# Kernel tuning notes

Hardware: AMD Instinct MI355X
Metric: run time of the kernel (lower is better)

Reference implementation:

```python
import jax, jax.numpy as jnp
import numpy as np

B, N, T, M, D, H = 2, 2048, 8, 256, 1024, 16
HD = D // H
EPS = 1e-5


def setup_inputs() -> dict:
    key = jax.random.key(0)
    ks = jax.random.split(key, 12)
    text_tokens = jax.random.normal(ks[0], (B, N, D), dtype=jnp.float32)
    media = jax.random.normal(ks[1], (B, T, M, D), dtype=jnp.float32)
    # exactly T media markers, evenly spaced, first at position 0 so no
    # fully-masked softmax row (matches well-formed usage of the module)
    loc = np.zeros((B, N), dtype=bool)
    loc[:, (np.arange(T) * (N // T))] = True
    media_locations = jnp.asarray(loc)
    s = 0.02
    return {
        "text_tokens": text_tokens,
        "media": media,
        "media_locations": media_locations,
        "ln_gamma": jnp.ones((D,), jnp.float32),
        "ln_beta": jnp.zeros((D,), jnp.float32),
        "wq": jax.random.normal(ks[2], (D, D), jnp.float32) * s,
        "wk": jax.random.normal(ks[3], (D, D), jnp.float32) * s,
        "wv": jax.random.normal(ks[4], (D, D), jnp.float32) * s,
        "bq": jnp.zeros((D,), jnp.float32),
        "bk": jnp.zeros((D,), jnp.float32),
        "bv": jnp.zeros((D,), jnp.float32),
        "w_out": jax.random.normal(ks[5], (D, D), jnp.float32) * s,
        "b_out": jnp.zeros((D,), jnp.float32),
    }


def _layernorm(x, gamma, beta):
    mu = jnp.mean(x, axis=-1, keepdims=True)
    var = jnp.mean(jnp.square(x - mu), axis=-1, keepdims=True)
    return (x - mu) * jax.lax.rsqrt(var + EPS) * gamma + beta


def reference(text_tokens, media, media_locations, ln_gamma, ln_beta,
              wq, wk, wv, bq, bk, bv, w_out, b_out):
    b, t, m, d = media.shape
    n = text_tokens.shape[1]
    h, hd = H, HD

    x = _layernorm(text_tokens, ln_gamma, ln_beta)          # [b,n,d]
    kv = media.reshape(b, t * m, d)                          # [b,tm,d]

    q = (x @ wq + bq).reshape(b, n, h, hd)
    k = (kv @ wk + bk).reshape(b, t * m, h, hd)
    v = (kv @ wv + bv).reshape(b, t * m, h, hd)

    scale = 1.0 / jnp.sqrt(jnp.asarray(hd, jnp.float32))
    scores = jnp.einsum('bnhk,bshk->bhns', q, k) * scale     # [b,h,n,tm]

    # media-locality mask: text token attends only to its immediately
    # preceding media frame (cumsum of media_locations == frame index)
    text_cumsum = jnp.cumsum(media_locations.astype(jnp.int32), axis=-1)  # [b,n]
    media_nums = jnp.repeat(jnp.arange(1, t + 1, dtype=jnp.int32), m)     # [tm]
    allowed = text_cumsum[:, :, None] == media_nums[None, None, :]        # [b,n,tm]
    scores = jnp.where(allowed[:, None, :, :], scores, -jnp.inf)

    attn = jax.nn.softmax(scores, axis=-1)                   # [b,h,n,tm]
    out = jnp.einsum('bhns,bshk->bnhk', attn, v).reshape(b, n, d)
    return out @ w_out + b_out
```

## Files before the change

kernel.cpp:

```cpp
#include <hip/hip_runtime.h>
#include <hip/hip_fp16.h>


typedef _Float16 h8 __attribute__((ext_vector_type(8)));
typedef _Float16 h4 __attribute__((ext_vector_type(4)));
typedef float f4 __attribute__((ext_vector_type(4)));

#define DI __device__ __forceinline__

DI void gload16(const void* g, void* l) {
  __builtin_amdgcn_global_load_lds((const __attribute__((address_space(1))) unsigned int*)g,
                                   (__attribute__((address_space(3))) unsigned int*)l, 16, 0, 0);
}

#define BAR() do { asm volatile("" ::: "memory"); __builtin_amdgcn_s_barrier(); asm volatile("" ::: "memory"); } while (0)

__global__ __launch_bounds__(256) void prep_kernel(
    const float* __restrict__ x, const float* __restrict__ gamma, const float* __restrict__ beta,
    _Float16* __restrict__ xh,
    const float* __restrict__ media, _Float16* __restrict__ kvh,
    const float* __restrict__ W0, const float* __restrict__ W1,
    const float* __restrict__ W2, const float* __restrict__ W3, _Float16* __restrict__ Wt,
    const int* __restrict__ locs, int* __restrict__ cnt, int* __restrict__ qlist) {
  int bid = blockIdx.x;
  int tid = threadIdx.x;
  if (bid < 4096) {
    int row = bid;
    const f4* xr = (const f4*)(x + (size_t)row * 1024);
    f4 v = xr[tid];
    float s = v[0] + v[1] + v[2] + v[3];
    float ss = v[0]*v[0] + v[1]*v[1] + v[2]*v[2] + v[3]*v[3];
    #pragma unroll
    for (int m = 1; m < 64; m <<= 1) { s += __shfl_xor(s, m); ss += __shfl_xor(ss, m); }
    __shared__ float red[8];
    int wid = tid >> 6, lane = tid & 63;
    if (lane == 0) { red[wid] = s; red[4 + wid] = ss; }
    __syncthreads();
    s = red[0] + red[1] + red[2] + red[3];
    ss = red[4] + red[5] + red[6] + red[7];
    float mean = s * (1.0f / 1024.0f);
    float var = ss * (1.0f / 1024.0f) - mean * mean;
    float rs = rsqrtf(var + 1e-5f);
    f4 g = ((const f4*)gamma)[tid], be = ((const f4*)beta)[tid];
    h4 o;
    #pragma unroll
    for (int j = 0; j < 4; ++j) o[j] = (_Float16)((v[j] - mean) * rs * g[j] + be[j]);
    ((h4*)(xh + (size_t)row * 1024))[tid] = o;
  } else if (bid < 8192) {
    int i = (bid - 4096) * 256 + tid;
    f4 v = ((const f4*)media)[i];
    h4 o;
    #pragma unroll
    for (int j = 0; j < 4; ++j) o[j] = (_Float16)v[j];
    ((h4*)kvh)[i] = o;
  } else if (bid < 12288) {
    int sec = bid - 8192;
    int z = sec >> 10, r = sec & 1023;
    const float* W = z == 0 ? W0 : z == 1 ? W1 : z == 2 ? W2 : W3;
    _Float16* out = Wt + (size_t)z * 1024 * 1024;
    __shared__ float tile[32][33];
    int i0 = (r & 31) * 32, o0 = (r >> 5) * 32;
    int tx = tid & 31, ty = tid >> 5;
    #pragma unroll
    for (int rr = 0; rr < 4; ++rr)
      tile[ty + rr * 8][tx] = W[(size_t)(i0 + ty + rr * 8) * 1024 + o0 + tx];
    __syncthreads();
    #pragma unroll
    for (int rr = 0; rr < 4; ++rr)
      out[(size_t)(o0 + ty + rr * 8) * 1024 + i0 + tx] = (_Float16)tile[tx][ty + rr * 8];
  } else {
    int b = bid - 12288;
    __shared__ int lcnt[8];
    if (tid < 8) lcnt[tid] = 0;
    __syncthreads();
    if (tid < 64) {
      int lane = tid;
      int run = 0; int v[32];
      #pragma unroll
      for (int i = 0; i < 32; ++i) { run += locs[b * 2048 + lane * 32 + i]; v[i] = run; }
      int incl = run;
      #pragma unroll
      for (int d = 1; d < 64; d <<= 1) { int t = __shfl_up(incl, d); if (lane >= d) incl += t; }
      int excl = incl - run;
      #pragma unroll
      for (int i = 0; i < 32; ++i) {
        int c = excl + v[i];
        if (c >= 1 && c <= 8) {
          int pos = atomicAdd(&lcnt[c - 1], 1);
          qlist[(b * 8 + (c - 1)) * 2048 + pos] = lane * 32 + i;
        }
      }
    }
    __syncthreads();
    if (tid < 8) cnt[b * 8 + tid] = lcnt[tid];
  }
}

struct GemmDesc { const _Float16* A; const _Float16* Bt; const float* bias; void* C; int mode; };
struct GemmBatch { GemmDesc d[3]; };

__global__ __launch_bounds__(512, 2) void gemm256(GemmBatch gb) {
  GemmDesc g = gb.d[blockIdx.z];
  int row0 = blockIdx.y * 256, col0 = blockIdx.x * 256;
  __shared__ alignas(16) _Float16 As[2][256 * 64];
  __shared__ alignas(16) _Float16 Bs[2][256 * 64];
  int tid = threadIdx.x, lane = tid & 63, wid = tid >> 6;
  int wr = wid >> 2, wc = wid & 3;
  int rs = tid >> 3;
  int cg = (tid & 7) ^ (rs & 7);
  const _Float16* gA = g.A + (size_t)(row0 + rs) * 1024 + cg * 8;
  const _Float16* gB = g.Bt + (size_t)(col0 + rs) * 1024 + cg * 8;
  int dstoff = wid * 8 * 64;
  f4 acc[8][4] = {};

  auto STAGE = [&](int kt, int buf) {
    #pragma unroll
    for (int s = 0; s < 4; ++s) {
      gload16(gA + (size_t)s * 65536 + kt * 64, (void*)&As[buf][s * 4096 + dstoff]);
      gload16(gB + (size_t)s * 65536 + kt * 64, (void*)&Bs[buf][s * 4096 + dstoff]);
    }
  };
  STAGE(0, 0);
  int c0 = (lane >> 4) ^ (lane & 7);
  int c1 = (4 + (lane >> 4)) ^ (lane & 7);
  #pragma unroll 1
  for (int t = 0; t < 16; ++t) {
    int buf = t & 1;
    BAR();
    if (t < 15) {
      STAGE(t + 1, buf ^ 1);
      asm volatile("s_waitcnt vmcnt(8)" ::: "memory");
    } else {
      asm volatile("s_waitcnt vmcnt(0)" ::: "memory");
    }
    BAR();
    #pragma unroll
    for (int kk = 0; kk < 2; ++kk) {
      int cc = kk ? c1 : c0;
      h8 a[8], b[4];
      #pragma unroll
      for (int m = 0; m < 8; ++m)
        a[m] = *(const h8*)&As[buf][(wr * 128 + m * 16 + (lane & 15)) * 64 + cc * 8];
      #pragma unroll
      for (int n = 0; n < 4; ++n)
        b[n] = *(const h8*)&Bs[buf][(wc * 64 + n * 16 + (lane & 15)) * 64 + cc * 8];
      __builtin_amdgcn_s_setprio(1);
      #pragma unroll
      for (int m = 0; m < 8; ++m)
        #pragma unroll
        for (int n = 0; n < 4; ++n)
          acc[m][n] = __builtin_amdgcn_mfma_f32_16x16x32_f16(a[m], b[n], acc[m][n], 0, 0, 0);
      __builtin_amdgcn_s_setprio(0);
    }
  }
  int colb = col0 + wc * 64;
  float bias_v[4];
  #pragma unroll
  for (int n = 0; n < 4; ++n) bias_v[n] = g.bias[colb + n * 16 + (lane & 15)];
  #pragma unroll
  for (int m = 0; m < 8; ++m) {
    int row = row0 + wr * 128 + m * 16 + (lane >> 4) * 4;
    #pragma unroll
    for (int n = 0; n < 4; ++n) {
      int col = colb + n * 16 + (lane & 15);
      if (g.mode == 0) {
        _Float16* C = (_Float16*)g.C;
        #pragma unroll
        for (int j = 0; j < 4; ++j)
          C[(size_t)(row + j) * 1024 + col] = (_Float16)(acc[m][n][j] + bias_v[n]);
      } else if (g.mode == 1) {
        float* C = (float*)g.C;
        #pragma unroll
        for (int j = 0; j < 4; ++j)
          C[(size_t)(row + j) * 1024 + col] = acc[m][n][j] + bias_v[n];
      } else {
        _Float16* C = (_Float16*)g.C;
        h4 pk;
        #pragma unroll
        for (int j = 0; j < 4; ++j) pk[j] = (_Float16)(acc[m][n][j] + bias_v[n]);
        size_t vrow = (size_t)((row >> 11) * 1024 + col);
        *(h4*)&C[vrow * 2048 + (row & 2047)] = pk;
      }
    }
  }
}

__global__ __launch_bounds__(512) void gemm128(GemmBatch gb) {
  GemmDesc g = gb.d[blockIdx.z];
  int row0 = blockIdx.y * 128, col0 = blockIdx.x * 128;
  __shared__ alignas(16) _Float16 As[128 * 64];
  __shared__ alignas(16) _Float16 Bs[128 * 64];
  int tid = threadIdx.x, lane = tid & 63, wid = tid >> 6;
  int wr = wid >> 2, wc = wid & 3;
  f4 acc[4][2] = {};
  int r0s = tid >> 3, c0s = tid & 7;
  int cg0 = c0s ^ (r0s & 7);
  int r1s = r0s + 64;
  int cg1 = c0s ^ (r1s & 7);
  const _Float16* gA0 = g.A + (size_t)(row0 + r0s) * 1024 + cg0 * 8;
  const _Float16* gA1 = g.A + (size_t)(row0 + r1s) * 1024 + cg1 * 8;
  const _Float16* gB0 = g.Bt + (size_t)(col0 + r0s) * 1024 + cg0 * 8;
  const _Float16* gB1 = g.Bt + (size_t)(col0 + r1s) * 1024 + cg1 * 8;
  #pragma unroll 1
  for (int kt = 0; kt < 16; ++kt) {
    __syncthreads();
    gload16(gA0 + kt * 64, (void*)&As[wid * 512]);
    gload16(gA1 + kt * 64, (void*)&As[4096 + wid * 512]);
    gload16(gB0 + kt * 64, (void*)&Bs[wid * 512]);
    gload16(gB1 + kt * 64, (void*)&Bs[4096 + wid * 512]);
    __syncthreads();
    h8 af[2][4], bf[2][2];
    #pragma unroll
    for (int kk = 0; kk < 2; ++kk) {
      #pragma unroll
      for (int m = 0; m < 4; ++m) {
        int r = wr * 64 + m * 16 + (lane & 15);
        int c = ((lane >> 4) + kk * 4) ^ (r & 7);
        af[kk][m] = *(const h8*)&As[r * 64 + c * 8];
      }
      #pragma unroll
      for (int n = 0; n < 2; ++n) {
        int r = wc * 32 + n * 16 + (lane & 15);
        int c = ((lane >> 4) + kk * 4) ^ (r & 7);
        bf[kk][n] = *(const h8*)&Bs[r * 64 + c * 8];
      }
    }
    #pragma unroll
    for (int kk = 0; kk < 2; ++kk)
      #pragma unroll
      for (int m = 0; m < 4; ++m)
        #pragma unroll
        for (int n = 0; n < 2; ++n)
          acc[m][n] = __builtin_amdgcn_mfma_f32_16x16x32_f16(af[kk][m], bf[kk][n], acc[m][n], 0, 0, 0);
  }
  int colb = col0 + wc * 32;
  float bias_v[2];
  #pragma unroll
  for (int n = 0; n < 2; ++n) bias_v[n] = g.bias[colb + n * 16 + (lane & 15)];
  #pragma unroll
  for (int m = 0; m < 4; ++m) {
    int row = row0 + wr * 64 + m * 16 + (lane >> 4) * 4;
    #pragma unroll
    for (int n = 0; n < 2; ++n) {
      int col = colb + n * 16 + (lane & 15);
      if (g.mode == 0) {
        _Float16* C = (_Float16*)g.C;
        #pragma unroll
        for (int j = 0; j < 4; ++j)
          C[(size_t)(row + j) * 1024 + col] = (_Float16)(acc[m][n][j] + bias_v[n]);
      } else if (g.mode == 1) {
        float* C = (float*)g.C;
        #pragma unroll
        for (int j = 0; j < 4; ++j)
          C[(size_t)(row + j) * 1024 + col] = acc[m][n][j] + bias_v[n];
      } else {
        _Float16* C = (_Float16*)g.C;
        h4 pk;
        #pragma unroll
        for (int j = 0; j < 4; ++j) pk[j] = (_Float16)(acc[m][n][j] + bias_v[n]);
        size_t vrow = (size_t)((row >> 11) * 1024 + col);
        *(h4*)&C[vrow * 2048 + (row & 2047)] = pk;
      }
    }
  }
}

__global__ __launch_bounds__(512) void attn_kernel(const _Float16* __restrict__ Qg,
    const _Float16* __restrict__ Kg, const _Float16* __restrict__ Vtg,
    const int* __restrict__ cnt, const int* __restrict__ qlist, _Float16* __restrict__ Og) {
  int h = blockIdx.x, f = blockIdx.y, b = blockIdx.z;
  __shared__ alignas(16) _Float16 Kl[256 * 64];
  __shared__ alignas(16) _Float16 Vl[64 * 256];
  __shared__ alignas(16) _Float16 Sl[8 * 16 * 256];
  int tid = threadIdx.x;
  for (int idx = tid; idx < 2048; idx += 512) {
    int r = idx >> 3, c = idx & 7;
    h8 v = *(const h8*)&Kg[((size_t)(b * 2048 + f * 256 + r)) * 1024 + h * 64 + c * 8];
    *(h8*)&Kl[r * 64 + ((c ^ (r & 7)) * 8)] = v;
  }
  for (int idx = tid; idx < 2048; idx += 512) {
    int d = idx >> 5, cc = idx & 31;
    h8 v = *(const h8*)&Vtg[((size_t)(b * 1024 + h * 64 + d)) * 2048 + f * 256 + cc * 8];
    *(h8*)&Vl[d * 256 + ((cc ^ (d & 7)) * 8)] = v;
  }
  __syncthreads();
  int nq = cnt[b * 8 + f];
  int lane = tid & 63, wid = tid >> 6;
  const int* ql = qlist + (b * 8 + f) * 2048;
  _Float16* Sw = &Sl[wid * 4096];
  for (int st = wid; st * 16 < nq; st += 8) {
    int qbase = st * 16;
    int nv = nq - qbase; if (nv > 16) nv = 16;
    int li = lane & 15; if (li > nv - 1) li = nv - 1;
    int qrow = b * 2048 + ql[qbase + li];
    h8 aq0 = *(const h8*)&Qg[(size_t)qrow * 1024 + h * 64 + (lane >> 4) * 8];
    h8 aq1 = *(const h8*)&Qg[(size_t)qrow * 1024 + h * 64 + 32 + (lane >> 4) * 8];
    f4 s[16];
    #pragma unroll
    for (int kt = 0; kt < 16; ++kt) {
      int key = kt * 16 + (lane & 15);
      int cb0 = lane >> 4;
      h8 bk0 = *(const h8*)&Kl[key * 64 + ((cb0 ^ (key & 7)) * 8)];
      h8 bk1 = *(const h8*)&Kl[key * 64 + (((cb0 + 4) ^ (key & 7)) * 8)];
      f4 z = {0.f, 0.f, 0.f, 0.f};
      s[kt] = __builtin_amdgcn_mfma_f32_16x16x32_f16(aq0, bk0, z, 0, 0, 0);
      s[kt] = __builtin_amdgcn_mfma_f32_16x16x32_f16(aq1, bk1, s[kt], 0, 0, 0);
    }
    float mx[4], sm[4];
    #pragma unroll
    for (int j = 0; j < 4; ++j) {
      float m = s[0][j];
      #pragma unroll
      for (int kt = 1; kt < 16; ++kt) m = fmaxf(m, s[kt][j]);
      #pragma unroll
      for (int d = 1; d < 16; d <<= 1) m = fmaxf(m, __shfl_xor(m, d));
      mx[j] = m; sm[j] = 0.f;
    }
    #pragma unroll
    for (int kt = 0; kt < 16; ++kt) {
      int keyb = kt * 16 + (lane & 15);
      int cbk = keyb >> 3, wi = keyb & 7;
      #pragma unroll
      for (int j = 0; j < 4; ++j) {
        float p = __expf((s[kt][j] - mx[j]) * 0.125f);
        sm[j] += p;
        int q = (lane >> 4) * 4 + j;
        Sw[q * 256 + ((cbk ^ (q & 7)) * 8) + wi] = (_Float16)p;
      }
    }
    #pragma unroll
    for (int j = 0; j < 4; ++j) {
      float x = sm[j];
      #pragma unroll
      for (int d = 1; d < 16; d <<= 1) x += __shfl_xor(x, d);
      sm[j] = x;
    }
    f4 o[4] = {};
    #pragma unroll
    for (int c32 = 0; c32 < 8; ++c32) {
      int qa = lane & 15;
      int cba = c32 * 4 + (lane >> 4);
      h8 pa = *(const h8*)&Sw[qa * 256 + ((cba ^ (qa & 7)) * 8)];
      #pragma unroll
      for (int dt = 0; dt < 4; ++dt) {
        int dd = dt * 16 + (lane & 15);
        h8 bv_ = *(const h8*)&Vl[dd * 256 + ((cba ^ (dd & 7)) * 8)];
        o[dt] = __builtin_amdgcn_mfma_f32_16x16x32_f16(pa, bv_, o[dt], 0, 0, 0);
      }
    }
    #pragma unroll
    for (int j = 0; j < 4; ++j) {
      int q = (lane >> 4) * 4 + j;
      if (q < nv) {
        int qr = __shfl(qrow, q);
        float inv = 1.0f / sm[j];
        #pragma unroll
        for (int dt = 0; dt < 4; ++dt)
          Og[(size_t)qr * 1024 + h * 64 + dt * 16 + (lane & 15)] = (_Float16)(o[dt][j] * inv);
      }
    }
  }
}

extern "C" void kernel_launch(void* const* d_in, const int* in_sizes, int n_in,
                              void* d_out, int out_size, void* d_ws, size_t ws_size,
                              hipStream_t stream) {
  const float* text  = (const float*)d_in[0];
  const float* media = (const float*)d_in[1];
  const int*   locs  = (const int*)d_in[2];
  const float* gamma = (const float*)d_in[3];
  const float* beta  = (const float*)d_in[4];
  const float* wq = (const float*)d_in[5];
  const float* wk = (const float*)d_in[6];
  const float* wv = (const float*)d_in[7];
  const float* bq = (const float*)d_in[8];
  const float* bk = (const float*)d_in[9];
  const float* bv = (const float*)d_in[10];
  const float* wo = (const float*)d_in[11];
  const float* bo = (const float*)d_in[12];

  char* ws = (char*)d_ws;
  size_t off = 0;
  auto take = [&](size_t bytes) { void* p = ws + off; off += (bytes + 255) & ~(size_t)255; return p; };
  _Float16* xh  = (_Float16*)take((size_t)4096 * 1024 * 2);
  _Float16* kvh = (_Float16*)take((size_t)4096 * 1024 * 2);
  _Float16* wt  = (_Float16*)take((size_t)4 * 1024 * 1024 * 2);
  _Float16* Qm  = (_Float16*)take((size_t)4096 * 1024 * 2);
  _Float16* Km  = (_Float16*)take((size_t)4096 * 1024 * 2);
  _Float16* Vt  = (_Float16*)take((size_t)2048 * 2048 * 2);
  _Float16* Om  = (_Float16*)take((size_t)4096 * 1024 * 2);
  int* cnt   = (int*)take(64 * sizeof(int));
  int* qlist = (int*)take((size_t)2 * 8 * 2048 * sizeof(int));

  prep_kernel<<<12290, 256, 0, stream>>>(text, gamma, beta, xh, media, kvh,
                                         wq, wk, wv, wo, wt, locs, cnt, qlist);

  GemmBatch gb;
  gb.d[0] = { xh,  wt,                       bq, (void*)Qm, 0 };
  gb.d[1] = { kvh, wt + (size_t)1 * 1048576, bk, (void*)Km, 0 };
  gb.d[2] = { kvh, wt + (size_t)2 * 1048576, bv, (void*)Vt, 2 };
  gemm256<<<dim3(4, 16, 3), 512, 0, stream>>>(gb);

  attn_kernel<<<dim3(16, 8, 2), 512, 0, stream>>>(Qm, Km, Vt, cnt, qlist, Om);

  GemmBatch gf;
  gf.d[0] = { Om, wt + (size_t)3 * 1048576, bo, d_out, 1 };
  gf.d[1] = gf.d[0];
  gf.d[2] = gf.d[0];
  gemm128<<<dim3(8, 32, 1), 512, 0, stream>>>(gf);
}
```

Baseline: 189.3 us.

## Interleave next-tile global loads with MFMA phases in gemm256 main loop

Restructures the 256x256 GEMM K-loop into four phases per K-tile. Each phase issues a quarter of the next tile's global-to-LDS loads, reads half the A fragments (B fragments once per k-half), and runs its MFMAs between barriers. The aim is to spread memory traffic across the compute and cut register pressure from holding all 8 A fragments, which may help occupancy at 2 blocks/CU. The trade-off is extra barriers per iteration and a full vmcnt(0) wait at the end of each tile.

```diff
diff --git a/kernel.cpp b/kernel.cpp
--- a/kernel.cpp
+++ b/kernel.cpp
@@ -110,56 +110,70 @@
   int cg = (tid & 7) ^ (rs & 7);
   const _Float16* gA = g.A + (size_t)(row0 + rs) * 1024 + cg * 8;
   const _Float16* gB = g.Bt + (size_t)(col0 + rs) * 1024 + cg * 8;
-  int dstoff = wid * 8 * 64;
   f4 acc[8][4] = {};
 
-  auto STAGE = [&](int kt, int buf) {
-    #pragma unroll
-    for (int s = 0; s < 4; ++s) {
-      gload16(gA + (size_t)s * 65536 + kt * 64, (void*)&As[buf][s * 4096 + dstoff]);
-      gload16(gB + (size_t)s * 65536 + kt * 64, (void*)&Bs[buf][s * 4096 + dstoff]);
+  auto STAGEG = [&](int kt, int buf, int grp) {
+    int s0 = (grp & 1) * 2;
+    if (grp < 2) {
+      gload16(gA + (size_t)s0 * 65536 + kt * 64,       (void*)&As[buf][s0 * 4096 + wid * 512]);
+      gload16(gA + (size_t)(s0 + 1) * 65536 + kt * 64, (void*)&As[buf][(s0 + 1) * 4096 + wid * 512]);
+    } else {
+      gload16(gB + (size_t)s0 * 65536 + kt * 64,       (void*)&Bs[buf][s0 * 4096 + wid * 512]);
+      gload16(gB + (size_t)(s0 + 1) * 65536 + kt * 64, (void*)&Bs[buf][(s0 + 1) * 4096 + wid * 512]);
     }
   };
-  STAGE(0, 0);
-  int c0 = (lane >> 4) ^ (lane & 7);
-  int c1 = (4 + (lane >> 4)) ^ (lane & 7);
+
+  #pragma unroll
+  for (int grp = 0; grp < 4; ++grp) STAGEG(0, 0, grp);
+  asm volatile("s_waitcnt vmcnt(0)" ::: "memory");
+  BAR();
+
+  h8 bfr[4];
   #pragma unroll 1
   for (int t = 0; t < 16; ++t) {
     int buf = t & 1;
-    BAR();
+    #pragma unroll
+    for (int ph = 0; ph < 4; ++ph) {
+      int kk = ph >> 1, mh = ph & 1;
+      if (t < 15) STAGEG(t + 1, buf ^ 1, ph);
+      if (mh == 0) {
+        #pragma unroll
+        for (int n = 0; n < 4; ++n) {
+          int r = wc * 64 + n * 16 + (lane & 15);
+          int c = ((lane >> 4) + kk * 4) ^ (r & 7);
+          bfr[n] = *(const h8*)&Bs[buf][r * 64 + c * 8];
+        }
+      }
+      h8 afr[4];
+      #pragma unroll
+      for (int m = 0; m < 4; ++m) {
+        int r = wr * 128 + mh * 64 + m * 16 + (lane & 15);
+        int c = ((lane >> 4) + kk * 4) ^ (r & 7);
+        afr[m] = *(const h8*)&As[buf][r * 64 + c * 8];
+      }
+      BAR();
+      __builtin_amdgcn_s_setprio(1);
+      #pragma unroll
+      for (int m = 0; m < 4; ++m)
+        #pragma unroll
+        for (int n = 0; n < 4; ++n)
+          acc[mh * 4 + m][n] = __builtin_amdgcn_mfma_f32_16x16x32_f16(afr[m], bfr[n], acc[mh * 4 + m][n], 0, 0, 0);
+      __builtin_amdgcn_s_setprio(0);
+      BAR();
+    }
     if (t < 15) {
-      STAGE(t + 1, buf ^ 1);
-      asm volatile("s_waitcnt vmcnt(8)" ::: "memory");
-    } else {
       asm volatile("s_waitcnt vmcnt(0)" ::: "memory");
-    }
-    BAR();
-    #pragma unroll
-    for (int kk = 0; kk < 2; ++kk) {
-      int cc = kk ? c1 : c0;
-      h8 a[8], b[4];
-      #pragma unroll
-      for (int m = 0; m < 8; ++m)
-        a[m] = *(const h8*)&As[buf][(wr * 128 + m * 16 + (lane & 15)) * 64 + cc * 8];
-      #pragma unroll
-      for (int n = 0; n < 4; ++n)
-        b[n] = *(const h8*)&Bs[buf][(wc * 64 + n * 16 + (lane & 15)) * 64 + cc * 8];
-      __builtin_amdgcn_s_setprio(1);
-      #pragma unroll
-      for (int m = 0; m < 8; ++m)
-        #pragma unroll
-        for (int n = 0; n < 4; ++n)
-          acc[m][n] = __builtin_amdgcn_mfma_f32_16x16x32_f16(a[m], b[n], acc[m][n], 0, 0, 0);
-      __builtin_amdgcn_s_setprio(0);
-    }
-  }
+      BAR();
+    }
+  }
+
   int colb = col0 + wc * 64;
   float bias_v[4];
   #pragma unroll
   for (int n = 0; n < 4; ++n) bias_v[n] = g.bias[colb + n * 16 + (lane & 15)];
   #pragma unroll
-  for (int m = 0; m < 8; ++m) {
-    int row = row0 + wr * 128 + m * 16 + (lane >> 4) * 4;
+  for (int mi = 0; mi < 8; ++mi) {
+    int row = row0 + wr * 128 + (mi >> 2) * 64 + (mi & 3) * 16 + (lane >> 4) * 4;
     #pragma unroll
     for (int n = 0; n < 4; ++n) {
       int col = colb + n * 16 + (lane & 15);
@@ -167,17 +181,17 @@
         _Float16* C = (_Float16*)g.C;
         #pragma unroll
         for (int j = 0; j < 4; ++j)
-          C[(size_t)(row + j) * 1024 + col] = (_Float16)(acc[m][n][j] + bias_v[n]);
+          C[(size_t)(row + j) * 1024 + col] = (_Float16)(acc[mi][n][j] + bias_v[n]);
       } else if (g.mode == 1) {
         float* C = (float*)g.C;
         #pragma unroll
         for (int j = 0; j < 4; ++j)
-          C[(size_t)(row + j) * 1024 + col] = acc[m][n][j] + bias_v[n];
+          C[(size_t)(row + j) * 1024 + col] = acc[mi][n][j] + bias_v[n];
       } else {
         _Float16* C = (_Float16*)g.C;
         h4 pk;
         #pragma unroll
-        for (int j = 0; j < 4; ++j) pk[j] = (_Float16)(acc[m][n][j] + bias_v[n]);
+        for (int j = 0; j < 4; ++j) pk[j] = (_Float16)(acc[mi][n][j] + bias_v[n]);
         size_t vrow = (size_t)((row >> 11) * 1024 + col);
         *(h4*)&C[vrow * 2048 + (row & 2047)] = pk;
       }
```

Result: slower. 205.9 us (+8.8%).
